# Optimization experiments

Measured on AMD Instinct MI355X. Metric: run time of the kernel, lower is better.

Reference implementation:

```python
import jax, jax.numpy as jnp
import numpy as np

T = 65536
OBS_DIM = 64
ACTION_DIM = 16
EMB_DIM = 8  # min(action_dim, 8)
HID = 256
NOBJ = 4
IN_DIM = OBS_DIM + EMB_DIM


def setup_inputs() -> dict:
    key = jax.random.key(0)
    ks = jax.random.split(key, 16)
    g = lambda k, shape, s=0.05: (jax.random.normal(k, shape, dtype=jnp.float32) * s)
    inp = {
        "observations": jax.random.normal(ks[0], (T, OBS_DIM), dtype=jnp.float32),
        "actions": jax.random.randint(ks[1], (T,), 0, ACTION_DIM),
        "emb": g(ks[2], (ACTION_DIM, EMB_DIM)),
        # layer 0 (input_dim -> hidden)
        "Win0": g(ks[3], (HID, IN_DIM)),
        "WB0": g(ks[4], (HID, IN_DIM)),
        "WC0": g(ks[5], (HID, IN_DIM)),
        "Wd0": g(ks[6], (HID, IN_DIM)),
        "Alog0": jax.random.normal(ks[7], (HID,), dtype=jnp.float32),
        # layer 1 (hidden -> hidden)
        "Win1": g(ks[8], (HID, HID)),
        "WB1": g(ks[9], (HID, HID)),
        "WC1": g(ks[10], (HID, HID)),
        "Wd1": g(ks[11], (HID, HID)),
        "Alog1": jax.random.normal(ks[12], (HID,), dtype=jnp.float32),
        # output head
        "Wout": g(ks[13], (NOBJ, HID)),
        "bout": jnp.zeros((NOBJ,), dtype=jnp.float32),
    }
    return inp


def _ssm_layer(x, Win, WB, WC, Wd, Alog):
    """One selective-SSM layer: h_t = exp(delta_t * A) * h_{t-1} + B_t * x_state_t; y = C * h."""
    x_state = x @ Win.T            # [T, H]
    B = x @ WB.T                   # [T, H]
    C = x @ WC.T                   # [T, H]
    delta = jax.nn.sigmoid(x @ Wd.T)  # [T, H]
    A = -jnp.exp(Alog)             # [H]
    A_bar = jnp.exp(delta * A)     # [T, H], decay factors
    Bx = B * x_state               # [T, H], inputs to the recurrence

    def step(h, inputs):
        a, bx = inputs
        h = a * h + bx
        return h, h

    h0 = jnp.zeros((x_state.shape[-1],), dtype=x_state.dtype)
    _, h_seq = jax.lax.scan(step, h0, (A_bar, Bx))
    return C * h_seq


def reference(observations, actions, emb,
              Win0, WB0, WC0, Wd0, Alog0,
              Win1, WB1, WC1, Wd1, Alog1,
              Wout, bout):
    x = jnp.concatenate([observations, emb[actions]], axis=-1)  # [T, IN_DIM]
    x = _ssm_layer(x, Win0, WB0, WC0, Wd0, Alog0)
    x = _ssm_layer(x, Win1, WB1, WC1, Wd1, Alog1)
    out = x @ Wout.T + bout                                     # [T, NOBJ]
    return jax.nn.softplus(out) + 1.0
```

## Files before the change

### kernel.cpp

```cpp
#include <hip/hip_runtime.h>

typedef unsigned short u16;
typedef __attribute__((ext_vector_type(8))) short bf16x8;
typedef __attribute__((ext_vector_type(4))) float f32x4;
typedef __attribute__((ext_vector_type(8))) unsigned short u16x8;

#define T_LEN 65536
#define HID 256
#define K0 96
#define K1 256
#define BM 128
#define BN 128
#define CHUNK 64
#define NCHUNK 1024
#define NSEG 32
#define CPS 32

__device__ __forceinline__ float bf2f(u16 u) {
  unsigned x = ((unsigned)u) << 16; float f; __builtin_memcpy(&f, &x, 4); return f;
}
__device__ __forceinline__ u16 f2bf(float f) {
  unsigned x; __builtin_memcpy(&x, &f, 4);
  x += 0x7FFFu + ((x >> 16) & 1u);
  return (u16)(x >> 16);
}

__device__ __forceinline__ void gl_lds16(const void* g, void* l) {
  __builtin_amdgcn_global_load_lds((const __attribute__((address_space(1))) unsigned int*)g,
                                   (__attribute__((address_space(3))) unsigned int*)l,
                                   16, 0, 0);
}

__global__ __launch_bounds__(256) void build_x0(
    const float* __restrict__ obs, const int* __restrict__ act,
    const float* __restrict__ emb, u16* __restrict__ x0)
{
  const int idx = blockIdx.x * 256 + threadIdx.x;
  const int t = idx / 24, seg = idx - t * 24;
  u16 v0 = 0, v1 = 0, v2 = 0, v3 = 0;
  if (seg < 16) {
    const float4 f = *(const float4*)&obs[(size_t)t * 64 + seg * 4];
    v0 = f2bf(f.x); v1 = f2bf(f.y); v2 = f2bf(f.z); v3 = f2bf(f.w);
  } else if (seg < 18) {
    const int a = act[t];
    const int e0 = (seg - 16) * 4;
    v0 = f2bf(emb[a * 8 + e0 + 0]); v1 = f2bf(emb[a * 8 + e0 + 1]);
    v2 = f2bf(emb[a * 8 + e0 + 2]); v3 = f2bf(emb[a * 8 + e0 + 3]);
  }
  u16* p = &x0[(size_t)t * 96 + seg * 4];
  p[0] = v0; p[1] = v1; p[2] = v2; p[3] = v3;
}

__global__ __launch_bounds__(256) void prep_w(
    const float* __restrict__ Win0, const float* __restrict__ WB0,
    const float* __restrict__ WC0,  const float* __restrict__ Wd0,
    const float* __restrict__ Alog0,
    const float* __restrict__ Win1, const float* __restrict__ WB1,
    const float* __restrict__ WC1,  const float* __restrict__ Wd1,
    const float* __restrict__ Alog1,
    u16* __restrict__ W0v, u16* __restrict__ W1v, float* __restrict__ Aneg)
{
  const int idx = blockIdx.x * 256 + threadIdx.x;
  if (idx < 1024 * K0) {
    const int row = idx / K0, k = idx - row * K0;
    const int p = (row >> 4) & 3;
    const int h = (row >> 6) * 16 + (row & 15);
    const float* W = (p == 0) ? Win0 : (p == 1) ? WB0 : (p == 2) ? WC0 : Wd0;
    W0v[idx] = f2bf((k < 72) ? W[h * 72 + k] : 0.f);
  } else if (idx < 1024 * K0 + 1024 * K1) {
    const int j = idx - 1024 * K0;
    const int row = j >> 8, k = j & 255;
    const int p = (row >> 4) & 3;
    const int h = (row >> 6) * 16 + (row & 15);
    const float* W = (p == 0) ? Win1 : (p == 1) ? WB1 : (p == 2) ? WC1 : Wd1;
    W1v[j] = f2bf(W[h * 256 + k]);
  } else if (idx < 1024 * K0 + 1024 * K1 + 512) {
    const int j = idx - (1024 * K0 + 1024 * K1);
    Aneg[j] = -__expf((j < 256) ? Alog0[j] : Alog1[j - 256]);
  }
}

template <int KDIM>
__global__ __launch_bounds__(256, 4) void gemm_scan(
    const u16* __restrict__ X, const u16* __restrict__ Wv,
    const float* __restrict__ Aneg,
    unsigned* __restrict__ uvb,
    float* __restrict__ aprod, float* __restrict__ hlast)
{
  static_assert(KDIM % 32 == 0, "K must be multiple of 32");
  constexpr int NK = KDIM / 32;
  __shared__ alignas(16) char smem[32768];

  const int tid = threadIdx.x;
  const int l   = tid & 63;
  const int w   = tid >> 6;
  const int bid = blockIdx.x;
  const int xcd = bid & 7;
  const int k_  = bid >> 3;
  const int mt  = xcd * 64 + (k_ >> 3);
  const int nt  = k_ & 7;
  const int m0  = mt * BM;
  const int n0  = nt * BN;
  const int wm  = (w >> 1) * 64;
  const int wn  = (w & 1) * 64;

  f32x4 acc[4][4];
  const f32x4 zero = {0.f, 0.f, 0.f, 0.f};
#pragma unroll
  for (int mi = 0; mi < 4; ++mi)
#pragma unroll
    for (int ni = 0; ni < 4; ++ni) acc[mi][ni] = zero;

  const int rr = w * 32 + (l >> 2);
  const int kb = (((l & 3) ^ ((l >> 3) & 3))) * 16;

#define STAGE(KS, BUF)                                                          \
  {                                                                             \
    _Pragma("unroll")                                                           \
    for (int i = 0; i < 2; ++i) {                                               \
      const char* gA = (const char*)(X + (size_t)(m0 + rr + i * 16) * KDIM + (KS) * 32) + kb; \
      gl_lds16(gA, smem + (BUF) * 16384 + w * 2048 + i * 1024);                 \
      const char* gB = (const char*)(Wv + (size_t)(n0 + rr + i * 16) * KDIM + (KS) * 32) + kb; \
      gl_lds16(gB, smem + (BUF) * 16384 + 8192 + w * 2048 + i * 1024);          \
    }                                                                           \
  }

  const int kgs = ((l >> 4) ^ ((l >> 1) & 3)) * 8;

  STAGE(0, 0);
  int cur = 0;
  for (int ks = 0; ks < NK; ++ks) {
    if (ks + 1 < NK) {
      STAGE(ks + 1, cur ^ 1);
      asm volatile("s_waitcnt vmcnt(4)" ::: "memory");
    } else {
      asm volatile("s_waitcnt vmcnt(0)" ::: "memory");
    }
    __builtin_amdgcn_s_barrier();
    asm volatile("" ::: "memory");

    const u16* sA = (const u16*)(smem + cur * 16384);
    const u16* sB = (const u16*)(smem + cur * 16384 + 8192);
    bf16x8 af[4], bfr[4];
#pragma unroll
    for (int mi = 0; mi < 4; ++mi)
      af[mi] = *(const bf16x8*)&sA[(wm + mi * 16 + (l & 15)) * 32 + kgs];
#pragma unroll
    for (int ni = 0; ni < 4; ++ni)
      bfr[ni] = *(const bf16x8*)&sB[(wn + ni * 16 + (l & 15)) * 32 + kgs];
#pragma unroll
    for (int mi = 0; mi < 4; ++mi)
#pragma unroll
      for (int ni = 0; ni < 4; ++ni)
        acc[mi][ni] = __builtin_amdgcn_mfma_f32_16x16x32_bf16(af[mi], bfr[ni], acc[mi][ni], 0, 0, 0);

    asm volatile("s_waitcnt lgkmcnt(0)" ::: "memory");
    __builtin_amdgcn_s_barrier();
    asm volatile("" ::: "memory");
    cur ^= 1;
  }
#undef STAGE

  const int lg = l >> 4;
  const int cc = l & 15;
  const int ch = (n0 >> 2) + (wn >> 6) * 16 + cc;
  const int chunk = mt * 2 + (wm >> 6);
  const float An = Aneg[ch];

  float Pl[4][4], Hl[4][4], Cv[4][4];
  float P3[4], H3[4];
#pragma unroll
  for (int mi = 0; mi < 4; ++mi) {
    float ap = 1.f, hl = 0.f;
#pragma unroll
    for (int v = 0; v < 4; ++v) {
      const float pin = acc[mi][0][v];
      const float pB  = acc[mi][1][v];
      const float pC  = acc[mi][2][v];
      const float pd  = acc[mi][3][v];
      const float delta = 1.f / (1.f + __expf(-pd));
      const float a  = __expf(delta * An);
      hl = a * hl + pB * pin;
      ap *= a;
      Pl[mi][v] = ap; Hl[mi][v] = hl; Cv[mi][v] = pC;
    }
    P3[mi] = ap; H3[mi] = hl;
  }

  float aL[4], hL[4], aT[4], hT[4];
#pragma unroll
  for (int mi = 0; mi < 4; ++mi) {
    float al = 1.f, hlx = 0.f, at = 1.f, ht = 0.f;
#pragma unroll
    for (int s = 0; s < 4; ++s) {
      const float Ab = __shfl(P3[mi], cc + s * 16, 64);
      const float Hb = __shfl(H3[mi], cc + s * 16, 64);
      if (s < lg) { hlx = Ab * hlx + Hb; al *= Ab; }
      ht = Ab * ht + Hb; at *= Ab;
    }
    aL[mi] = al; hL[mi] = hlx; aT[mi] = at; hT[mi] = ht;
  }

  unsigned* ub = uvb + ((size_t)bid * 4 + w) * 1024;
  float aM = 1.f, hM = 0.f;
#pragma unroll
  for (int mi = 0; mi < 4; ++mi) {
    const float a_pre = aL[mi] * aM;
    const float h_pre = aL[mi] * hM + hL[mi];
#pragma unroll
    for (int v = 0; v < 4; ++v) {
      const float Pt = Pl[mi][v] * a_pre;
      const float Ht = Pl[mi][v] * h_pre + Hl[mi][v];
      const unsigned pack = (unsigned)f2bf(Cv[mi][v] * Ht)
                          | ((unsigned)f2bf(Cv[mi][v] * Pt) << 16);
      ub[(mi * 4 + v) * 64 + l] = pack;
    }
    hM = aT[mi] * hM + hT[mi];
    aM *= aT[mi];
  }
  if (lg == 0) {
    aprod[(size_t)chunk * HID + ch] = aM;
    hlast[(size_t)chunk * HID + ch] = hM;
  }
}

__global__ __launch_bounds__(256) void pass2a(
    const float* __restrict__ aprod, const float* __restrict__ hlast,
    float* __restrict__ clocal, float* __restrict__ apfxc,
    float* __restrict__ segAP, float* __restrict__ segHL)
{
  const int s = blockIdx.x;
  const int h = threadIdx.x;
  float H = 0.f, P = 1.f;
#pragma unroll 4
  for (int j = 0; j < CPS; ++j) {
    const size_t o = (size_t)(s * CPS + j) * HID + h;
    clocal[o] = H; apfxc[o] = P;
    const float a = aprod[o], hh = hlast[o];
    H = a * H + hh;
    P *= a;
  }
  segAP[s * HID + h] = P;
  segHL[s * HID + h] = H;
}

__global__ __launch_bounds__(256) void pass2b(
    const float* __restrict__ segAP, const float* __restrict__ segHL,
    float* __restrict__ segc)
{
  const int h = threadIdx.x;
  float S = 0.f;
#pragma unroll 4
  for (int s = 0; s < NSEG; ++s) {
    segc[s * HID + h] = S;
    S = segAP[s * HID + h] * S + segHL[s * HID + h];
  }
}

__global__ __launch_bounds__(256) void combine(
    const unsigned* __restrict__ uvb,
    const float* __restrict__ clocal, const float* __restrict__ apfxc,
    const float* __restrict__ segc, u16* __restrict__ y)
{
  const size_t vi = (size_t)blockIdx.x * 256 + threadIdx.x;
  const int t   = (int)(vi >> 5);
  const int ch0 = ((int)vi & 31) * 8;
  const int ck  = t >> 6;
  const int sg  = ck / CPS;
  const float* cl = &clocal[(size_t)ck * HID + ch0];
  const float* ax = &apfxc[(size_t)ck * HID + ch0];
  const float* sc = &segc[(size_t)sg * HID + ch0];
  const float4 cl0 = *(const float4*)&cl[0], cl1 = *(const float4*)&cl[4];
  const float4 ax0 = *(const float4*)&ax[0], ax1 = *(const float4*)&ax[4];
  const float4 sc0 = *(const float4*)&sc[0], sc1 = *(const float4*)&sc[4];
  const float crv[8] = {
    cl0.x + ax0.x * sc0.x, cl0.y + ax0.y * sc0.y,
    cl0.z + ax0.z * sc0.z, cl0.w + ax0.w * sc0.w,
    cl1.x + ax1.x * sc1.x, cl1.y + ax1.y * sc1.y,
    cl1.z + ax1.z * sc1.z, cl1.w + ax1.w * sc1.w };
  const int mt = t >> 7, tt = t & 127;
  const int wmh = tt >> 6, mi = (tt >> 4) & 3, lg = (tt >> 2) & 3, v = tt & 3;
  const int nt = ch0 >> 5, ch5 = ch0 & 31, wnh = ch5 >> 4, cc0 = ch5 & 15;
  const int w = wmh * 2 + wnh;
  const int bid = (((mt & 63) * 8 + nt) << 3) | (mt >> 6);
  const unsigned* up = uvb + ((size_t)bid * 4 + w) * 1024 + (mi * 4 + v) * 64
                           + lg * 16 + cc0;
  const uint4 p0 = *(const uint4*)&up[0];
  const uint4 p1 = *(const uint4*)&up[4];
  const unsigned pk[8] = {p0.x, p0.y, p0.z, p0.w, p1.x, p1.y, p1.z, p1.w};
  u16x8 o;
#pragma unroll
  for (int j = 0; j < 8; ++j)
    o[j] = f2bf(bf2f((u16)(pk[j] & 0xffffu)) + bf2f((u16)(pk[j] >> 16)) * crv[j]);
  *(u16x8*)&y[vi * 8] = o;
}

__global__ __launch_bounds__(256) void head(
    const u16* __restrict__ y1, const float* __restrict__ Wout,
    const float* __restrict__ bout, float* __restrict__ out)
{
  __shared__ u16 ly[64 * 264];
  __shared__ float lw[4 * HID];
  __shared__ float lb[4];
  const int tid = threadIdx.x;
  for (int i = tid; i < 4 * HID; i += 256) lw[i] = Wout[i];
  if (tid < 4) lb[tid] = bout[tid];
  const size_t rbase = (size_t)blockIdx.x * 64 * HID;
#pragma unroll
  for (int i = 0; i < 8; ++i) {
    const int lin = i * 256 + tid;
    const int r = lin >> 5, c8 = lin & 31;
    *(u16x8*)&ly[r * 264 + c8 * 8] = *(const u16x8*)&y1[rbase + (size_t)r * HID + c8 * 8];
  }
  __syncthreads();
  const int t = tid >> 2, o = tid & 3;
  float acc = lb[o];
#pragma unroll 8
  for (int h = 0; h < HID; ++h)
    acc += bf2f(ly[t * 264 + h]) * lw[o * HID + h];
  out[((size_t)blockIdx.x * 64 + t) * 4 + o] = logf(1.f + __expf(acc)) + 1.f;
}

extern "C" void kernel_launch(void* const* d_in, const int* in_sizes, int n_in,
                              void* d_out, int out_size, void* d_ws, size_t ws_size,
                              hipStream_t stream)
{
  (void)in_sizes; (void)n_in; (void)out_size; (void)ws_size;
  const float* obs   = (const float*)d_in[0];
  const int*   act   = (const int*)d_in[1];
  const float* emb   = (const float*)d_in[2];
  const float* Win0  = (const float*)d_in[3];
  const float* WB0   = (const float*)d_in[4];
  const float* WC0   = (const float*)d_in[5];
  const float* Wd0   = (const float*)d_in[6];
  const float* Alog0 = (const float*)d_in[7];
  const float* Win1  = (const float*)d_in[8];
  const float* WB1   = (const float*)d_in[9];
  const float* WC1   = (const float*)d_in[10];
  const float* Wd1   = (const float*)d_in[11];
  const float* Alog1 = (const float*)d_in[12];
  const float* Wout  = (const float*)d_in[13];
  const float* bout  = (const float*)d_in[14];
  float* out = (float*)d_out;

  char* ws = (char*)d_ws;
  size_t off = 0;
  auto alloc = [&](size_t bytes) {
    char* p = ws + off;
    off += (bytes + 255) & ~(size_t)255;
    return p;
  };
  u16*      x0    = (u16*)     alloc((size_t)T_LEN * K0 * 2);
  u16*      W0v   = (u16*)     alloc((size_t)1024 * K0 * 2);
  u16*      W1v   = (u16*)     alloc((size_t)1024 * K1 * 2);
  float*    Aneg  = (float*)   alloc(512 * 4);
  unsigned* uvb   = (unsigned*)alloc((size_t)T_LEN * HID * 4);
  u16*      y     = (u16*)     alloc((size_t)T_LEN * HID * 2);
  float*    aprod = (float*)   alloc((size_t)NCHUNK * HID * 4);
  float*    hlast = (float*)   alloc((size_t)NCHUNK * HID * 4);
  float*    clocal= (float*)   alloc((size_t)NCHUNK * HID * 4);
  float*    apfxc = (float*)   alloc((size_t)NCHUNK * HID * 4);
  float*    segAP = (float*)   alloc((size_t)NSEG * HID * 4);
  float*    segHL = (float*)   alloc((size_t)NSEG * HID * 4);
  float*    segc  = (float*)   alloc((size_t)NSEG * HID * 4);

  build_x0<<<T_LEN * 24 / 256, 256, 0, stream>>>(obs, act, emb, x0);
  prep_w<<<(1024 * K0 + 1024 * K1 + 512 + 255) / 256, 256, 0, stream>>>(
      Win0, WB0, WC0, Wd0, Alog0, Win1, WB1, WC1, Wd1, Alog1, W0v, W1v, Aneg);

  gemm_scan<K0><<<4096, 256, 0, stream>>>(x0, W0v, Aneg, uvb, aprod, hlast);
  pass2a<<<NSEG, 256, 0, stream>>>(aprod, hlast, clocal, apfxc, segAP, segHL);
  pass2b<<<1, 256, 0, stream>>>(segAP, segHL, segc);
  combine<<<T_LEN * HID / 8 / 256, 256, 0, stream>>>(uvb, clocal, apfxc, segc, y);

  gemm_scan<K1><<<4096, 256, 0, stream>>>(y, W1v, Aneg + 256, uvb, aprod, hlast);
  pass2a<<<NSEG, 256, 0, stream>>>(aprod, hlast, clocal, apfxc, segAP, segHL);
  pass2b<<<1, 256, 0, stream>>>(segAP, segHL, segc);
  combine<<<T_LEN * HID / 8 / 256, 256, 0, stream>>>(uvb, clocal, apfxc, segc, y);

  head<<<T_LEN / 64, 256, 0, stream>>>(y, Wout, bout, out);
}
```

Baseline: 251.3 us.

## Triple-buffer GEMM K-loop loads and merge input/weight prep kernels

The GEMM+scan kernel moves from double to triple buffering of LDS tiles, prefetching two K-steps ahead with adjusted vmcnt waits, and the K loop is fully unrolled. This raises LDS use to 48KB and lowers the launch-bounds occupancy hint from 4 to 3 blocks per CU. The two prep kernels (input build and weight conversion) are merged into one launch to save a kernel launch. The risk is lower occupancy offsetting the deeper prefetch, since NK is small (3 or 8).

```diff
diff --git a/kernel.cpp b/kernel.cpp
--- a/kernel.cpp
+++ b/kernel.cpp
@@ -31,36 +31,37 @@
                                    16, 0, 0);
 }
 
-__global__ __launch_bounds__(256) void build_x0(
+#define NX (T_LEN * 24)
+__global__ __launch_bounds__(256) void prep_all(
     const float* __restrict__ obs, const int* __restrict__ act,
-    const float* __restrict__ emb, u16* __restrict__ x0)
-{
-  const int idx = blockIdx.x * 256 + threadIdx.x;
-  const int t = idx / 24, seg = idx - t * 24;
-  u16 v0 = 0, v1 = 0, v2 = 0, v3 = 0;
-  if (seg < 16) {
-    const float4 f = *(const float4*)&obs[(size_t)t * 64 + seg * 4];
-    v0 = f2bf(f.x); v1 = f2bf(f.y); v2 = f2bf(f.z); v3 = f2bf(f.w);
-  } else if (seg < 18) {
-    const int a = act[t];
-    const int e0 = (seg - 16) * 4;
-    v0 = f2bf(emb[a * 8 + e0 + 0]); v1 = f2bf(emb[a * 8 + e0 + 1]);
-    v2 = f2bf(emb[a * 8 + e0 + 2]); v3 = f2bf(emb[a * 8 + e0 + 3]);
-  }
-  u16* p = &x0[(size_t)t * 96 + seg * 4];
-  p[0] = v0; p[1] = v1; p[2] = v2; p[3] = v3;
-}
-
-__global__ __launch_bounds__(256) void prep_w(
+    const float* __restrict__ emb,
     const float* __restrict__ Win0, const float* __restrict__ WB0,
     const float* __restrict__ WC0,  const float* __restrict__ Wd0,
     const float* __restrict__ Alog0,
     const float* __restrict__ Win1, const float* __restrict__ WB1,
     const float* __restrict__ WC1,  const float* __restrict__ Wd1,
     const float* __restrict__ Alog1,
-    u16* __restrict__ W0v, u16* __restrict__ W1v, float* __restrict__ Aneg)
-{
-  const int idx = blockIdx.x * 256 + threadIdx.x;
+    u16* __restrict__ x0, u16* __restrict__ W0v, u16* __restrict__ W1v,
+    float* __restrict__ Aneg)
+{
+  int idx = blockIdx.x * 256 + threadIdx.x;
+  if (idx < NX) {
+    const int t = idx / 24, seg = idx - t * 24;
+    u16 v0 = 0, v1 = 0, v2 = 0, v3 = 0;
+    if (seg < 16) {
+      const float4 f = *(const float4*)&obs[(size_t)t * 64 + seg * 4];
+      v0 = f2bf(f.x); v1 = f2bf(f.y); v2 = f2bf(f.z); v3 = f2bf(f.w);
+    } else if (seg < 18) {
+      const int a = act[t];
+      const int e0 = (seg - 16) * 4;
+      v0 = f2bf(emb[a * 8 + e0 + 0]); v1 = f2bf(emb[a * 8 + e0 + 1]);
+      v2 = f2bf(emb[a * 8 + e0 + 2]); v3 = f2bf(emb[a * 8 + e0 + 3]);
+    }
+    u16* p = &x0[(size_t)t * 96 + seg * 4];
+    p[0] = v0; p[1] = v1; p[2] = v2; p[3] = v3;
+    return;
+  }
+  idx -= NX;
   if (idx < 1024 * K0) {
     const int row = idx / K0, k = idx - row * K0;
     const int p = (row >> 4) & 3;
@@ -81,7 +82,7 @@
 }
 
 template <int KDIM>
-__global__ __launch_bounds__(256, 4) void gemm_scan(
+__global__ __launch_bounds__(256, 3) void gemm_scan(
     const u16* __restrict__ X, const u16* __restrict__ Wv,
     const float* __restrict__ Aneg,
     unsigned* __restrict__ uvb,
@@ -89,7 +90,7 @@
 {
   static_assert(KDIM % 32 == 0, "K must be multiple of 32");
   constexpr int NK = KDIM / 32;
-  __shared__ alignas(16) char smem[32768];
+  __shared__ alignas(16) char smem[49152];
 
   const int tid = threadIdx.x;
   const int l   = tid & 63;
@@ -128,19 +129,19 @@
   const int kgs = ((l >> 4) ^ ((l >> 1) & 3)) * 8;
 
   STAGE(0, 0);
-  int cur = 0;
+  if (NK > 1) STAGE(1, 1);
+#pragma unroll
   for (int ks = 0; ks < NK; ++ks) {
-    if (ks + 1 < NK) {
-      STAGE(ks + 1, cur ^ 1);
-      asm volatile("s_waitcnt vmcnt(4)" ::: "memory");
-    } else {
-      asm volatile("s_waitcnt vmcnt(0)" ::: "memory");
-    }
+    if (ks + 2 < NK) STAGE(ks + 2, (ks + 2) % 3);
+    const int rem = NK - 1 - ks;
+    if (rem >= 2)      asm volatile("s_waitcnt vmcnt(8)" ::: "memory");
+    else if (rem == 1) asm volatile("s_waitcnt vmcnt(4)" ::: "memory");
+    else               asm volatile("s_waitcnt vmcnt(0)" ::: "memory");
     __builtin_amdgcn_s_barrier();
     asm volatile("" ::: "memory");
 
-    const u16* sA = (const u16*)(smem + cur * 16384);
-    const u16* sB = (const u16*)(smem + cur * 16384 + 8192);
+    const u16* sA = (const u16*)(smem + (ks % 3) * 16384);
+    const u16* sB = (const u16*)(smem + (ks % 3) * 16384 + 8192);
     bf16x8 af[4], bfr[4];
 #pragma unroll
     for (int mi = 0; mi < 4; ++mi)
@@ -157,7 +158,6 @@
     asm volatile("s_waitcnt lgkmcnt(0)" ::: "memory");
     __builtin_amdgcn_s_barrier();
     asm volatile("" ::: "memory");
-    cur ^= 1;
   }
 #undef STAGE
 
@@ -364,9 +364,11 @@
   float*    segHL = (float*)   alloc((size_t)NSEG * HID * 4);
   float*    segc  = (float*)   alloc((size_t)NSEG * HID * 4);
 
-  build_x0<<<T_LEN * 24 / 256, 256, 0, stream>>>(obs, act, emb, x0);
-  prep_w<<<(1024 * K0 + 1024 * K1 + 512 + 255) / 256, 256, 0, stream>>>(
-      Win0, WB0, WC0, Wd0, Alog0, Win1, WB1, WC1, Wd1, Alog1, W0v, W1v, Aneg);
+  const int prep_threads = NX + 1024 * K0 + 1024 * K1 + 512;
+  prep_all<<<(prep_threads + 255) / 256, 256, 0, stream>>>(
+      obs, act, emb,
+      Win0, WB0, WC0, Wd0, Alog0, Win1, WB1, WC1, Wd1, Alog1,
+      x0, W0v, W1v, Aneg);
 
   gemm_scan<K0><<<4096, 256, 0, stream>>>(x0, W0v, Aneg, uvb, aprod, hlast);
   pass2a<<<NSEG, 256, 0, stream>>>(aprod, hlast, clocal, apfxc, segAP, segHL);
```

Result: faster. 244.1 us (-2.9%).
